# Optimization experiments

Measured on AMD Instinct MI355X. Metric: run time of the kernel, lower is better.

## Reference

```python
import jax, jax.numpy as jnp
import numpy as np

B, H, W = 8, 48, 48
D_MODEL, D_STATE, SSM_RATIO, K = 192, 16, 2.0, 4
D_INNER = int(SSM_RATIO * D_MODEL)        # 384
DT_RANK = int(np.ceil(D_MODEL / 16))       # 12
EPS = 1e-6


def setup_inputs() -> dict:
    key = jax.random.key(0)
    ks = jax.random.split(key, 12)
    s = 0.02
    inp = {
        "x": jax.random.normal(ks[0], (B, H, W, D_MODEL), jnp.float32),
        "in_proj_w": s * jax.random.normal(ks[1], (2 * D_INNER, D_MODEL), jnp.float32),
        "conv_w": s * jax.random.normal(ks[2], (D_INNER, 1, 3, 3), jnp.float32),
        "conv_b": jnp.zeros((D_INNER,), jnp.float32),
        "x_proj_w": s * jax.random.normal(ks[3], (K, DT_RANK + 2 * D_STATE, D_INNER), jnp.float32),
        "dt_w": s * jax.random.normal(ks[4], (K, D_INNER, DT_RANK), jnp.float32),
        "dt_bias": 0.05 * jax.random.normal(ks[5], (K, D_INNER), jnp.float32),
        "A_logs": jnp.log(jnp.broadcast_to(jnp.arange(1, D_STATE + 1, dtype=jnp.float32), (K * D_INNER, D_STATE)).copy()),
        "Ds": jnp.ones((K * D_INNER,), jnp.float32),
        "ln_w": jnp.ones((D_INNER,), jnp.float32),
        "ln_b": jnp.zeros((D_INNER,), jnp.float32),
        "out_proj_w": s * jax.random.normal(ks[6], (D_MODEL, D_INNER), jnp.float32),
    }
    return inp


def _selective_scan(u, dt, A, Bs, Cs):
    # u, dt: (B,K,D,L); A: (K,D,N); Bs, Cs: (B,K,N,L)
    u_t = jnp.moveaxis(u, -1, 0)    # (L,B,K,D)
    dt_t = jnp.moveaxis(dt, -1, 0)  # (L,B,K,D)
    B_t = jnp.moveaxis(Bs, -1, 0)   # (L,B,K,N)
    C_t = jnp.moveaxis(Cs, -1, 0)   # (L,B,K,N)
    b = u.shape[0]
    h0 = jnp.zeros((b, K, D_INNER, D_STATE), jnp.float32)

    def step(h, inp):
        ut, dtt, bt, ct = inp
        dA = jnp.exp(dtt[..., None] * A)                       # (B,K,D,N)
        h = dA * h + (dtt * ut)[..., None] * bt[:, :, None, :]  # (B,K,D,N)
        y = jnp.einsum('bkdn,bkn->bkd', h, ct)
        return h, y

    _, ys = jax.lax.scan(step, h0, (u_t, dt_t, B_t, C_t))
    return jnp.moveaxis(ys, 0, -1)  # (B,K,D,L)


def reference(x, in_proj_w, conv_w, conv_b, x_proj_w, dt_w, dt_bias, A_logs, Ds, ln_w, ln_b, out_proj_w):
    b, h, w, _ = x.shape
    L = h * w
    # in_proj + split into x / gate z
    xz = jnp.einsum('bhwc,oc->bhwo', x, in_proj_w)
    xi, z = jnp.split(xz, 2, axis=-1)
    z = jax.nn.silu(z)
    # depthwise 3x3 conv, channel-first
    xi = jnp.transpose(xi, (0, 3, 1, 2))  # (B,Di,H,W)
    xi = jax.lax.conv_general_dilated(
        xi, conv_w, window_strides=(1, 1), padding='SAME',
        feature_group_count=D_INNER,
        dimension_numbers=('NCHW', 'OIHW', 'NCHW')) + conv_b[None, :, None, None]
    xi = jax.nn.silu(xi)
    # cross-scan: 4 directions (row-major, col-major, and their reverses)
    xr = xi.reshape(b, D_INNER, L)
    xc = jnp.transpose(xi, (0, 1, 3, 2)).reshape(b, D_INNER, L)
    xs = jnp.stack([xr, xc, jnp.flip(xr, -1), jnp.flip(xc, -1)], axis=1)  # (B,K,D,L)
    # per-direction projections
    x_dbl = jnp.einsum('bkdl,kcd->bkcl', xs, x_proj_w)  # (B,K,R+2N,L)
    dts = x_dbl[:, :, :DT_RANK]
    Bs = x_dbl[:, :, DT_RANK:DT_RANK + D_STATE]
    Cs = x_dbl[:, :, DT_RANK + D_STATE:]
    dts = jnp.einsum('bkrl,kdr->bkdl', dts, dt_w)
    A = -jnp.exp(A_logs.astype(jnp.float32)).reshape(K, D_INNER, D_STATE)
    dt = jax.nn.softplus(dts + dt_bias[None, :, :, None])
    ys = _selective_scan(xs.astype(jnp.float32), dt, A, Bs.astype(jnp.float32), Cs.astype(jnp.float32))
    ys = ys + Ds.reshape(1, K, D_INNER, 1) * xs  # skip
    # cross-merge (invert each direction, sum)
    def col2row(t):
        return jnp.transpose(t.reshape(b, D_INNER, w, h), (0, 1, 3, 2)).reshape(b, D_INNER, L)
    y = ys[:, 0] + col2row(ys[:, 1]) + jnp.flip(ys[:, 2], -1) + col2row(jnp.flip(ys[:, 3], -1))
    y = jnp.transpose(y.reshape(b, D_INNER, h, w), (0, 2, 3, 1))  # (B,H,W,Di)
    # LayerNorm over channel dim
    mu = y.mean(-1, keepdims=True)
    var = ((y - mu) ** 2).mean(-1, keepdims=True)
    y = (y - mu) / jnp.sqrt(var + EPS) * ln_w + ln_b
    # gate + out_proj
    y = y * z
    out = jnp.einsum('bhwd,od->bhwo', y, out_proj_w)
    return out.astype(x.dtype)
```

## Files before the change

kernel.cpp:

```cpp
#include <hip/hip_runtime.h>

#define BB 8
#define HH 48
#define WW2 48
#define LL 2304
#define CIN 192
#define DI 384
#define NK 4
#define RR 12
#define NS 16
#define CD 44
#define NX 176
#define MM 18432
#define NC 48
#define CL 48

typedef unsigned short u16;
typedef __attribute__((ext_vector_type(8))) short s16x8;
typedef __attribute__((ext_vector_type(4))) float f32x4;
typedef __attribute__((ext_vector_type(2))) float f32x2;

#if __has_builtin(__builtin_elementwise_fma)
#define EFMA(a, b, c) __builtin_elementwise_fma((a), (b), (c))
#else
#define EFMA(a, b, c) ((a) * (b) + (c))
#endif

static __device__ __forceinline__ float siluf(float x) { return x / (1.f + __expf(-x)); }

static __device__ __forceinline__ u16 f2bf(float x) {
    unsigned u = __float_as_uint(x);
    return (u16)((u + 0x7FFFu + ((u >> 16) & 1u)) >> 16);
}
static __device__ __forceinline__ float bf2f(u16 h) {
    return __uint_as_float(((unsigned)h) << 16);
}

static __device__ __forceinline__ int posmap(int k, int l) {
    switch (k & 3) {
    case 0: return l;
    case 1: { int w = l / HH; int h = l - w * HH; return h * WW2 + w; }
    case 2: return LL - 1 - l;
    default: { int j = LL - 1 - l; int w = j / HH; int h = j - w * HH; return h * WW2 + w; }
    }
}

#define W0N 147456
#define W1N 67584
#define W2N 73728
__global__ __launch_bounds__(256) void k_cvtw(const float* __restrict__ w0,
                                              const float* __restrict__ w1,
                                              const float* __restrict__ w2,
                                              u16* __restrict__ wpl) {
    int i = (blockIdx.x * 256 + threadIdx.x) * 4;
    const float* src; u16* hi; u16* lo; int base;
    if (i < W0N)                { src = w0; hi = wpl;          lo = wpl + 147456; base = i; }
    else if (i < W0N + W1N)     { src = w1; hi = wpl + 294912; lo = wpl + 362496; base = i - W0N; }
    else if (i < W0N + W1N + W2N) { src = w2; hi = wpl + 430080; lo = wpl + 503808; base = i - W0N - W1N; }
    else return;
    float4 v = *(const float4*)(src + base);
    u16 h0 = f2bf(v.x), h1 = f2bf(v.y), h2 = f2bf(v.z), h3 = f2bf(v.w);
    hi[base + 0] = h0; hi[base + 1] = h1; hi[base + 2] = h2; hi[base + 3] = h3;
    lo[base + 0] = f2bf(v.x - bf2f(h0));
    lo[base + 1] = f2bf(v.y - bf2f(h1));
    lo[base + 2] = f2bf(v.z - bf2f(h2));
    lo[base + 3] = f2bf(v.w - bf2f(h3));
}

template<int N, int K, int EPI, int ACVT, int SPLIT>
__global__ __launch_bounds__(256) void k_gemm(const u16* __restrict__ Ahg,
                                              const u16* __restrict__ Alg,
                                              const u16* __restrict__ Bhg,
                                              const u16* __restrict__ Blg,
                                              float* __restrict__ O1,
                                              void* __restrict__ O2) {
    __shared__ __align__(16) u16 lds[SPLIT == 3 ? 12288 : 10240];
    const int m0 = blockIdx.x << 7;
    const int n0 = blockIdx.y << 6;
    const int t = threadIdx.x;
    const int lane = t & 63;
    const int w = t >> 6;
    const int wm = w & 1, wn = w >> 1;

    f32x4 acc[4][2];
#pragma unroll
    for (int mi = 0; mi < 4; ++mi)
#pragma unroll
        for (int ni = 0; ni < 2; ++ni)
#pragma unroll
            for (int r = 0; r < 4; ++r) acc[mi][ni][r] = 0.f;

    const int rA = lane & 15;
    const int kb = (lane >> 4) << 3;

    for (int k0 = 0; k0 < K; k0 += 32) {
#pragma unroll
        for (int rep = 0; rep < 2; ++rep) {
            int q = t + (rep << 8);
            int row = q >> 2;
            int kk = (q & 3) << 3;
            size_t ga = (size_t)(m0 + row) * K + k0 + kk;
            if (ACVT) {
                const float* Af = (const float*)Ahg;
                float vv[8];
                *(float4*)(vv + 0) = *(const float4*)(Af + ga);
                *(float4*)(vv + 4) = *(const float4*)(Af + ga + 4);
                u16 hbuf[8], lbuf[8];
#pragma unroll
                for (int i = 0; i < 8; ++i) {
                    u16 h = f2bf(vv[i]);
                    hbuf[i] = h;
                    lbuf[i] = f2bf(vv[i] - bf2f(h));
                }
                *(uint4*)&lds[(row << 5) + kk] = *(uint4*)hbuf;
                *(uint4*)&lds[4096 + (row << 5) + kk] = *(uint4*)lbuf;
            } else {
                *(uint4*)&lds[(row << 5) + kk] = *(const uint4*)(Ahg + ga);
                *(uint4*)&lds[4096 + (row << 5) + kk] = *(const uint4*)(Alg + ga);
            }
        }
        {
            int row = t >> 2;
            int kk = (t & 3) << 3;
            int rg = n0 + row;
            if (N & 63) rg = (rg > N - 1) ? (N - 1) : rg;
            size_t gb = (size_t)rg * K + k0 + kk;
            *(uint4*)&lds[8192 + (row << 5) + kk] = *(const uint4*)(Bhg + gb);
            if (SPLIT == 3)
                *(uint4*)&lds[10240 + (row << 5) + kk] = *(const uint4*)(Blg + gb);
        }
        __syncthreads();

        s16x8 bh[2], bl[2];
#pragma unroll
        for (int ni = 0; ni < 2; ++ni) {
            int c = (wn << 5) + (ni << 4) + rA;
            bh[ni] = *(const s16x8*)&lds[8192 + (c << 5) + kb];
            if (SPLIT == 3) bl[ni] = *(const s16x8*)&lds[10240 + (c << 5) + kb];
        }
#pragma unroll
        for (int mi = 0; mi < 4; ++mi) {
            int rr = (wm << 6) + (mi << 4) + rA;
            s16x8 ah = *(const s16x8*)&lds[(rr << 5) + kb];
            s16x8 al = *(const s16x8*)&lds[4096 + (rr << 5) + kb];
#pragma unroll
            for (int ni = 0; ni < 2; ++ni) {
                acc[mi][ni] = __builtin_amdgcn_mfma_f32_16x16x32_bf16(al, bh[ni], acc[mi][ni], 0, 0, 0);
                if (SPLIT == 3)
                    acc[mi][ni] = __builtin_amdgcn_mfma_f32_16x16x32_bf16(ah, bl[ni], acc[mi][ni], 0, 0, 0);
                acc[mi][ni] = __builtin_amdgcn_mfma_f32_16x16x32_bf16(ah, bh[ni], acc[mi][ni], 0, 0, 0);
            }
        }
        __syncthreads();
    }

    const int rbase = (lane >> 4) << 2;
#pragma unroll
    for (int mi = 0; mi < 4; ++mi) {
#pragma unroll
        for (int ni = 0; ni < 2; ++ni) {
            int o = n0 + (wn << 5) + (ni << 4) + (lane & 15);
#pragma unroll
            for (int r = 0; r < 4; ++r) {
                int m = m0 + (wm << 6) + (mi << 4) + rbase + r;
                float v = acc[mi][ni][r];
                if (EPI == 0) {
                    if (o < DI) O1[(size_t)m * DI + o] = v;
                    else        ((u16*)O2)[(size_t)m * DI + (o - DI)] = f2bf(siluf(v));
                } else if (EPI == 1) {
                    if (o < NX) O1[(size_t)m * NX + o] = v;
                } else {
                    O1[(size_t)m * CIN + o] = v;
                }
            }
        }
    }
}

__global__ __launch_bounds__(192) void k_conv(const float* __restrict__ xi,
                                              const float* __restrict__ cw,
                                              const float* __restrict__ cb,
                                              float* __restrict__ ub,
                                              u16* __restrict__ ubh,
                                              u16* __restrict__ ubl) {
    int blk = blockIdx.x;
    int b = blk / LL, p = blk - b * LL;
    int h = p / WW2, w = p - h * WW2;
    int d2 = threadIdx.x * 2;

    float w0[9], w1[9];
#pragma unroll
    for (int i = 0; i < 9; ++i) {
        w0[i] = cw[d2 * 9 + i];
        w1[i] = cw[(d2 + 1) * 9 + i];
    }
    float ax = cb[d2], ay = cb[d2 + 1];
#pragma unroll
    for (int dh = -1; dh <= 1; ++dh) {
        int hh = h + dh;
        if (hh < 0 || hh >= HH) continue;
#pragma unroll
        for (int dw = -1; dw <= 1; ++dw) {
            int ww = w + dw;
            if (ww < 0 || ww >= WW2) continue;
            float2 v = *(const float2*)(xi + ((size_t)b * LL + hh * WW2 + ww) * DI + d2);
            int tap = (dh + 1) * 3 + (dw + 1);
            ax = fmaf(w0[tap], v.x, ax);
            ay = fmaf(w1[tap], v.y, ay);
        }
    }
    float ox = siluf(ax), oy = siluf(ay);
    size_t idx = ((size_t)b * LL + p) * DI + d2;
    float2 o2; o2.x = ox; o2.y = oy;
    *(float2*)(ub + idx) = o2;
    u16 h0 = f2bf(ox), h1 = f2bf(oy);
    *(unsigned*)(ubh + idx) = (unsigned)h0 | ((unsigned)h1 << 16);
    unsigned l0 = f2bf(ox - bf2f(h0)), l1 = f2bf(oy - bf2f(h1));
    *(unsigned*)(ubl + idx) = l0 | (l1 << 16);
}

static __device__ __forceinline__ void adv_p(int k, int& p, int& hh) {
    if (k == 0) { ++p; }
    else if (k == 2) { --p; }
    else if (k == 1) {
        bool wrap = (hh == HH - 1);
        hh = wrap ? 0 : hh + 1;
        p += wrap ? -(LL - 1 - HH) : WW2;
    } else {
        bool wrap = (hh == 0);
        hh = wrap ? HH - 1 : hh - 1;
        p += wrap ? (LL - 1 - HH) : -WW2;
    }
}

static __device__ __forceinline__ void init_p(int k, int l0, int& p, int& hh) {
    hh = 0;
    if (k == 0) p = l0;
    else if (k == 2) p = LL - 1 - l0;
    else if (k == 1) { int w0 = l0 / HH; hh = l0 - w0 * HH; p = hh * WW2 + w0; }
    else { int j0 = LL - 1 - l0; int w0 = j0 / HH; hh = j0 - w0 * HH; p = hh * WW2 + w0; }
}

static __device__ __forceinline__ void scan_decode(int blk, int& b, int& k, int& dblk, int& c) {
    b = blk & 7;
    int r = blk >> 3;
    c = r % NC;
    int t2 = r / NC;
    dblk = t2 % 3;
    k = t2 / 3;
}

__global__ __launch_bounds__(128) void k_scan1(const float* __restrict__ ub,
                                               const float* __restrict__ xdbl,
                                               const float* __restrict__ dt_w,
                                               const float* __restrict__ dt_bias,
                                               const float* __restrict__ A_logs,
                                               float* __restrict__ HF,
                                               float* __restrict__ SD) {
    int b, k, dblk, c;
    scan_decode(blockIdx.x, b, k, dblk, c);
    int bk = (b << 2) | k;
    int d = (dblk << 7) + threadIdx.x;
    int kd = k * DI + d;

    float dtw[RR];
#pragma unroll
    for (int r = 0; r < RR; ++r) dtw[r] = dt_w[(size_t)kd * RR + r];
    float dtb = dt_bias[kd];
    float a[NS];
    bool fast = true;
#pragma unroll
    for (int n = 0; n < NS; ++n) {
        a[n] = -__expf(A_logs[(size_t)kd * NS + n]);
        fast = fast && (fabsf(a[n] + (float)(n + 1)) < 1e-3f * (float)(n + 1));
    }
    int use_fast = __all((int)fast);

    f32x2 h2[8];
#pragma unroll
    for (int i = 0; i < 8; ++i) { h2[i][0] = 0.f; h2[i][1] = 0.f; }
    float sumdt = 0.f;

    const float* cb0 = xdbl + (size_t)b * LL * NX + k * CD;
    const float* ubase = ub + (size_t)b * LL * DI + d;
    const int l0 = c * CL;
    int p, hh;
    init_p(k, l0, p, hh);

    if (use_fast) {
        for (int li = 0; li < CL; ++li) {
            const float4* cp4 = (const float4*)(cb0 + (size_t)p * NX);
            float dq[12];
            *(float4*)(dq + 0) = cp4[0];
            *(float4*)(dq + 4) = cp4[1];
            *(float4*)(dq + 8) = cp4[2];
            float s = dtb;
#pragma unroll
            for (int r = 0; r < RR; ++r) s = fmaf(dtw[r], dq[r], s);
            float es = __expf(s);
            float dt = (s > 15.f) ? s : __logf(1.f + es);
            float E = __builtin_amdgcn_rcpf(1.f + es);
            sumdt += dt;
            float uv = ubase[(size_t)p * DI];
            float du = dt * uv;
            float bb2[16];
            *(float4*)(bb2 + 0)  = cp4[3];
            *(float4*)(bb2 + 4)  = cp4[4];
            *(float4*)(bb2 + 8)  = cp4[5];
            *(float4*)(bb2 + 12) = cp4[6];
            const f32x2* b2 = (const f32x2*)bb2;
            float ee = E * E;
            f32x2 pw2; pw2[0] = E; pw2[1] = ee;
            f32x2 ee2; ee2[0] = ee; ee2[1] = ee;
            f32x2 du2; du2[0] = du; du2[1] = du;
#pragma unroll
            for (int i = 0; i < 8; ++i) {
                h2[i] = EFMA(du2, b2[i], pw2 * h2[i]);
                if (i < 7) pw2 = pw2 * ee2;
            }
            adv_p(k, p, hh);
        }
    } else {
        for (int li = 0; li < CL; ++li) {
            int l = l0 + li;
            int pp = posmap(k, l);
            const float* cp = cb0 + (size_t)pp * NX;
            float s = dtb;
#pragma unroll
            for (int r = 0; r < RR; ++r) s = fmaf(dtw[r], cp[r], s);
            float dt = (s > 15.f) ? s : log1pf(__expf(s));
            sumdt += dt;
            float uv = ubase[(size_t)pp * DI];
            float du = dt * uv;
#pragma unroll
            for (int n = 0; n < NS; ++n) {
                float dA = __expf(dt * a[n]);
                float hv = h2[n >> 1][n & 1];
                h2[n >> 1][n & 1] = fmaf(du, cp[RR + n], dA * hv);
            }
        }
    }
    size_t base = ((size_t)bk * NC + c);
#pragma unroll
    for (int i = 0; i < 8; ++i) {
        HF[(base * NS + 2 * i) * DI + d] = h2[i][0];
        HF[(base * NS + 2 * i + 1) * DI + d] = h2[i][1];
    }
    SD[base * DI + d] = sumdt;
}

__global__ __launch_bounds__(256) void k_scan2(const float* __restrict__ A_logs,
                                               float* __restrict__ HF,
                                               const float* __restrict__ SD) {
    int idx = blockIdx.x * 256 + threadIdx.x;
    int bk = idx / DI;
    int d = idx - bk * DI;
    int k = bk & 3;
    int kd = k * DI + d;

    float a[NS];
    bool fast = true;
#pragma unroll
    for (int n = 0; n < NS; ++n) {
        a[n] = -__expf(A_logs[(size_t)kd * NS + n]);
        fast = fast && (fabsf(a[n] + (float)(n + 1)) < 1e-3f * (float)(n + 1));
    }
    int use_fast = __all((int)fast);

    float H[NS];
#pragma unroll
    for (int n = 0; n < NS; ++n) H[n] = 0.f;

    for (int c = 0; c < NC; ++c) {
        size_t base = ((size_t)bk * NC + c);
        float sd = SD[base * DI + d];
        if (use_fast) {
            float E = __expf(-sd);
            float pw = 1.f;
#pragma unroll
            for (int n = 0; n < NS; ++n) {
                pw *= E;
                float hf = HF[(base * NS + n) * DI + d];
                HF[(base * NS + n) * DI + d] = H[n];
                H[n] = fmaf(pw, H[n], hf);
            }
        } else {
#pragma unroll
            for (int n = 0; n < NS; ++n) {
                float dec = __expf(a[n] * sd);
                float hf = HF[(base * NS + n) * DI + d];
                HF[(base * NS + n) * DI + d] = H[n];
                H[n] = fmaf(dec, H[n], hf);
            }
        }
    }
}

__global__ __launch_bounds__(128) void k_scan3(const float* __restrict__ ub,
                                               const float* __restrict__ xdbl,
                                               const float* __restrict__ dt_w,
                                               const float* __restrict__ dt_bias,
                                               const float* __restrict__ A_logs,
                                               const float* __restrict__ Ds,
                                               const float* __restrict__ HF,
                                               float* __restrict__ ycomb) {
    int b, k, dblk, c;
    scan_decode(blockIdx.x, b, k, dblk, c);
    int bk = (b << 2) | k;
    int d = (dblk << 7) + threadIdx.x;
    int kd = k * DI + d;

    float dtw[RR];
#pragma unroll
    for (int r = 0; r < RR; ++r) dtw[r] = dt_w[(size_t)kd * RR + r];
    float dtb = dt_bias[kd];
    float dsv = Ds[kd];
    float a[NS];
    bool fast = true;
#pragma unroll
    for (int n = 0; n < NS; ++n) {
        a[n] = -__expf(A_logs[(size_t)kd * NS + n]);
        fast = fast && (fabsf(a[n] + (float)(n + 1)) < 1e-3f * (float)(n + 1));
    }
    int use_fast = __all((int)fast);

    f32x2 h2[8];
    size_t sbase = ((size_t)bk * NC + c);
#pragma unroll
    for (int i = 0; i < 8; ++i) {
        h2[i][0] = HF[(sbase * NS + 2 * i) * DI + d];
        h2[i][1] = HF[(sbase * NS + 2 * i + 1) * DI + d];
    }

    const float* cb0 = xdbl + (size_t)b * LL * NX + k * CD;
    const float* ubase = ub + (size_t)b * LL * DI + d;
    float* ybase = ycomb + (size_t)b * LL * DI + d;
    const int l0 = c * CL;
    int p, hh;
    init_p(k, l0, p, hh);

    if (use_fast) {
        for (int li = 0; li < CL; ++li) {
            const float4* cp4 = (const float4*)(cb0 + (size_t)p * NX);
            float dq[12];
            *(float4*)(dq + 0) = cp4[0];
            *(float4*)(dq + 4) = cp4[1];
            *(float4*)(dq + 8) = cp4[2];
            float s = dtb;
#pragma unroll
            for (int r = 0; r < RR; ++r) s = fmaf(dtw[r], dq[r], s);
            float es = __expf(s);
            float dt = (s > 15.f) ? s : __logf(1.f + es);
            float E = __builtin_amdgcn_rcpf(1.f + es);
            float uv = ubase[(size_t)p * DI];
            float du = dt * uv;
            float bc[32];
            *(float4*)(bc + 0)  = cp4[3];
            *(float4*)(bc + 4)  = cp4[4];
            *(float4*)(bc + 8)  = cp4[5];
            *(float4*)(bc + 12) = cp4[6];
            *(float4*)(bc + 16) = cp4[7];
            *(float4*)(bc + 20) = cp4[8];
            *(float4*)(bc + 24) = cp4[9];
            *(float4*)(bc + 28) = cp4[10];
            const f32x2* b2 = (const f32x2*)bc;
            float ee = E * E;
            f32x2 pw2; pw2[0] = E; pw2[1] = ee;
            f32x2 ee2; ee2[0] = ee; ee2[1] = ee;
            f32x2 du2; du2[0] = du; du2[1] = du;
            f32x2 y2; y2[0] = 0.f; y2[1] = 0.f;
#pragma unroll
            for (int i = 0; i < 8; ++i) {
                h2[i] = EFMA(du2, b2[i], pw2 * h2[i]);
                y2 = EFMA(h2[i], b2[8 + i], y2);
                if (i < 7) pw2 = pw2 * ee2;
            }
            atomicAdd(ybase + (size_t)p * DI, fmaf(dsv, uv, y2[0] + y2[1]));
            adv_p(k, p, hh);
        }
    } else {
        for (int li = 0; li < CL; ++li) {
            int l = l0 + li;
            int pp = posmap(k, l);
            const float* cp = cb0 + (size_t)pp * NX;
            float s = dtb;
#pragma unroll
            for (int r = 0; r < RR; ++r) s = fmaf(dtw[r], cp[r], s);
            float dt = (s > 15.f) ? s : log1pf(__expf(s));
            float uv = ubase[(size_t)pp * DI];
            float du = dt * uv;
            float y = 0.f;
#pragma unroll
            for (int n = 0; n < NS; ++n) {
                float dA = __expf(dt * a[n]);
                float hv = h2[n >> 1][n & 1];
                hv = fmaf(du, cp[RR + n], dA * hv);
                h2[n >> 1][n & 1] = hv;
                y = fmaf(hv, cp[RR + NS + n], y);
            }
            atomicAdd(ybase + (size_t)pp * DI, fmaf(dsv, uv, y));
        }
    }
}

static __device__ __forceinline__ float waveRedSum(float v) {
#pragma unroll
    for (int o = 32; o; o >>= 1) v += __shfl_down(v, o);
    return v;
}

__global__ __launch_bounds__(128) void k_lngate(const float* __restrict__ ycomb,
                                                const u16* __restrict__ zb16,
                                                const float* __restrict__ lnw,
                                                const float* __restrict__ lnb,
                                                u16* __restrict__ ylnh,
                                                u16* __restrict__ ylnl) {
    int m = blockIdx.x;
    const float* yr = ycomb + (size_t)m * DI;
    float v[3];
    float s1 = 0.f, s2 = 0.f;
#pragma unroll
    for (int i = 0; i < 3; ++i) {
        v[i] = yr[threadIdx.x + (i << 7)];
        s1 += v[i];
        s2 = fmaf(v[i], v[i], s2);
    }
    s1 = waveRedSum(s1);
    s2 = waveRedSum(s2);
    __shared__ float p1[2], p2[2];
    int wid = threadIdx.x >> 6, lane = threadIdx.x & 63;
    if (lane == 0) { p1[wid] = s1; p2[wid] = s2; }
    __syncthreads();
    float S1 = p1[0] + p1[1];
    float S2 = p2[0] + p2[1];
    float mu = S1 * (1.f / DI);
    float var = S2 * (1.f / DI) - mu * mu;
    float rstd = rsqrtf(var + 1e-6f);
#pragma unroll
    for (int i = 0; i < 3; ++i) {
        int dd = threadIdx.x + (i << 7);
        float o = ((v[i] - mu) * rstd) * lnw[dd] + lnb[dd];
        float g = o * bf2f(zb16[(size_t)m * DI + dd]);
        u16 hh = f2bf(g);
        ylnh[(size_t)m * DI + dd] = hh;
        ylnl[(size_t)m * DI + dd] = f2bf(g - bf2f(hh));
    }
}

extern "C" void kernel_launch(void* const* d_in, const int* in_sizes, int n_in,
                              void* d_out, int out_size, void* d_ws, size_t ws_size,
                              hipStream_t stream) {
    const float* x         = (const float*)d_in[0];
    const float* in_proj_w = (const float*)d_in[1];
    const float* conv_w    = (const float*)d_in[2];
    const float* conv_b    = (const float*)d_in[3];
    const float* x_proj_w  = (const float*)d_in[4];
    const float* dt_w      = (const float*)d_in[5];
    const float* dt_bias   = (const float*)d_in[6];
    const float* A_logs    = (const float*)d_in[7];
    const float* Ds        = (const float*)d_in[8];
    const float* ln_w      = (const float*)d_in[9];
    const float* ln_b      = (const float*)d_in[10];
    const float* out_proj_w= (const float*)d_in[11];
    float* out = (float*)d_out;
    float* ws  = (float*)d_ws;

    const size_t SZ = (size_t)MM * DI;
    float* xi    = ws;
    u16*   zb16  = (u16*)(ws + SZ + SZ / 2);
    float* ub    = ws + 2 * SZ;
    float* xdbl  = ws + 3 * SZ;
    float* ycomb = ws + 3 * SZ + (size_t)MM * NX;
    u16*   wpl   = (u16*)(ycomb + SZ);

    u16* wphi  = wpl;
    u16* wplo  = wpl + 147456;
    u16* xpwhi = wpl + 294912;
    u16* xpwlo = wpl + 362496;
    u16* wohi  = wpl + 430080;
    u16* wolo  = wpl + 503808;

    u16* ubh  = (u16*)ycomb; u16* ubl = ubh + SZ;
    u16* ylnh = (u16*)xi;  u16* ylnl = ylnh + SZ;
    float* HF = ws;
    float* SD = ws + (size_t)BB * NK * NC * NS * DI;

    k_cvtw<<<(W0N + W1N + W2N) / 4 / 256 + 1, 256, 0, stream>>>(in_proj_w, x_proj_w, out_proj_w, wpl);

    k_gemm<768, CIN, 0, 1, 2><<<dim3(MM / 128, 12), 256, 0, stream>>>(
        (const u16*)x, nullptr, wphi, wplo, xi, (void*)zb16);

    k_conv<<<MM, 192, 0, stream>>>(xi, conv_w, conv_b, ub, ubh, ubl);

    k_gemm<NX, DI, 1, 0, 2><<<dim3(MM / 128, 3), 256, 0, stream>>>(ubh, ubl, xpwhi, xpwlo, xdbl, nullptr);

    hipMemsetAsync(ycomb, 0, SZ * sizeof(float), stream);

    const int nscan = BB * NK * 3 * NC;
    k_scan1<<<nscan, 128, 0, stream>>>(ub, xdbl, dt_w, dt_bias, A_logs, HF, SD);
    k_scan2<<<BB * NK * DI / 256, 256, 0, stream>>>(A_logs, HF, SD);
    k_scan3<<<nscan, 128, 0, stream>>>(ub, xdbl, dt_w, dt_bias, A_logs, Ds, HF, ycomb);

    k_lngate<<<MM, 128, 0, stream>>>(ycomb, zb16, ln_w, ln_b, ylnh, ylnl);

    k_gemm<CIN, DI, 2, 0, 2><<<dim3(MM / 128, 3), 256, 0, stream>>>(ylnh, ylnl, wohi, wolo, out, nullptr);
}
```

Measured before the change: 322.6 us.

## Fuse LayerNorm-apply and gating into out_proj GEMM A-operand load

Replaces the lngate kernel, which wrote hi/lo bf16 copies of the normalized, gated activations, with a small stats kernel that writes only per-row mean and rstd. The out_proj GEMM now reads fp32 ycomb and bf16 z directly and applies LayerNorm, affine and gate while splitting into hi/lo in its A-tile load. This removes a full write and reread of two bf16 activation buffers. In exchange the normalization work is repeated in each of the 3 N-tile blocks and the A loads become wider fp32 plus z reads.

```diff
diff --git a/kernel.cpp b/kernel.cpp
--- a/kernel.cpp
+++ b/kernel.cpp
@@ -73,7 +73,10 @@
                                               const u16* __restrict__ Bhg,
                                               const u16* __restrict__ Blg,
                                               float* __restrict__ O1,
-                                              void* __restrict__ O2) {
+                                              void* __restrict__ O2,
+                                              const float* __restrict__ lnw,
+                                              const float* __restrict__ lnb,
+                                              const float* __restrict__ stats) {
     __shared__ __align__(16) u16 lds[SPLIT == 3 ? 12288 : 10240];
     const int m0 = blockIdx.x << 7;
     const int n0 = blockIdx.y << 6;
@@ -100,7 +103,7 @@
             int row = q >> 2;
             int kk = (q & 3) << 3;
             size_t ga = (size_t)(m0 + row) * K + k0 + kk;
-            if (ACVT) {
+            if (ACVT == 1) {
                 const float* Af = (const float*)Ahg;
                 float vv[8];
                 *(float4*)(vv + 0) = *(const float4*)(Af + ga);
@@ -111,6 +114,30 @@
                     u16 h = f2bf(vv[i]);
                     hbuf[i] = h;
                     lbuf[i] = f2bf(vv[i] - bf2f(h));
+                }
+                *(uint4*)&lds[(row << 5) + kk] = *(uint4*)hbuf;
+                *(uint4*)&lds[4096 + (row << 5) + kk] = *(uint4*)lbuf;
+            } else if (ACVT == 2) {
+                const float* Yf = (const float*)Ahg;
+                int m = m0 + row;
+                float mu = stats[2 * m], rs = stats[2 * m + 1];
+                float vv[8];
+                *(float4*)(vv + 0) = *(const float4*)(Yf + ga);
+                *(float4*)(vv + 4) = *(const float4*)(Yf + ga + 4);
+                uint4 zz4 = *(const uint4*)(Alg + ga);
+                const u16* zz = (const u16*)&zz4;
+                float lw[8], lb[8];
+                *(float4*)(lw + 0) = *(const float4*)(lnw + k0 + kk);
+                *(float4*)(lw + 4) = *(const float4*)(lnw + k0 + kk + 4);
+                *(float4*)(lb + 0) = *(const float4*)(lnb + k0 + kk);
+                *(float4*)(lb + 4) = *(const float4*)(lnb + k0 + kk + 4);
+                u16 hbuf[8], lbuf[8];
+#pragma unroll
+                for (int i = 0; i < 8; ++i) {
+                    float g = fmaf((vv[i] - mu) * rs, lw[i], lb[i]) * bf2f(zz[i]);
+                    u16 h = f2bf(g);
+                    hbuf[i] = h;
+                    lbuf[i] = f2bf(g - bf2f(h));
                 }
                 *(uint4*)&lds[(row << 5) + kk] = *(uint4*)hbuf;
                 *(uint4*)&lds[4096 + (row << 5) + kk] = *(uint4*)lbuf;
@@ -503,47 +530,28 @@
     }
 }
 
-static __device__ __forceinline__ float waveRedSum(float v) {
-#pragma unroll
-    for (int o = 32; o; o >>= 1) v += __shfl_down(v, o);
-    return v;
-}
-
-__global__ __launch_bounds__(128) void k_lngate(const float* __restrict__ ycomb,
-                                                const u16* __restrict__ zb16,
-                                                const float* __restrict__ lnw,
-                                                const float* __restrict__ lnb,
-                                                u16* __restrict__ ylnh,
-                                                u16* __restrict__ ylnl) {
-    int m = blockIdx.x;
+__global__ __launch_bounds__(256) void k_lnstat(const float* __restrict__ ycomb,
+                                                float* __restrict__ stats) {
+    int m = blockIdx.x * 4 + (threadIdx.x >> 6);
+    int lane = threadIdx.x & 63;
     const float* yr = ycomb + (size_t)m * DI;
-    float v[3];
     float s1 = 0.f, s2 = 0.f;
 #pragma unroll
-    for (int i = 0; i < 3; ++i) {
-        v[i] = yr[threadIdx.x + (i << 7)];
-        s1 += v[i];
-        s2 = fmaf(v[i], v[i], s2);
-    }
-    s1 = waveRedSum(s1);
-    s2 = waveRedSum(s2);
-    __shared__ float p1[2], p2[2];
-    int wid = threadIdx.x >> 6, lane = threadIdx.x & 63;
-    if (lane == 0) { p1[wid] = s1; p2[wid] = s2; }
-    __syncthreads();
-    float S1 = p1[0] + p1[1];
-    float S2 = p2[0] + p2[1];
-    float mu = S1 * (1.f / DI);
-    float var = S2 * (1.f / DI) - mu * mu;
-    float rstd = rsqrtf(var + 1e-6f);
-#pragma unroll
-    for (int i = 0; i < 3; ++i) {
-        int dd = threadIdx.x + (i << 7);
-        float o = ((v[i] - mu) * rstd) * lnw[dd] + lnb[dd];
-        float g = o * bf2f(zb16[(size_t)m * DI + dd]);
-        u16 hh = f2bf(g);
-        ylnh[(size_t)m * DI + dd] = hh;
-        ylnl[(size_t)m * DI + dd] = f2bf(g - bf2f(hh));
+    for (int i = 0; i < 6; ++i) {
+        float v = yr[lane + (i << 6)];
+        s1 += v;
+        s2 = fmaf(v, v, s2);
+    }
+#pragma unroll
+    for (int o = 32; o; o >>= 1) {
+        s1 += __shfl_down(s1, o);
+        s2 += __shfl_down(s2, o);
+    }
+    if (lane == 0) {
+        float mu = s1 * (1.f / DI);
+        float var = s2 * (1.f / DI) - mu * mu;
+        stats[2 * m] = mu;
+        stats[2 * m + 1] = rsqrtf(var + 1e-6f);
     }
 }
 
@@ -581,18 +589,19 @@
     u16* wolo  = wpl + 503808;
 
     u16* ubh  = (u16*)ycomb; u16* ubl = ubh + SZ;
-    u16* ylnh = (u16*)xi;  u16* ylnl = ylnh + SZ;
     float* HF = ws;
     float* SD = ws + (size_t)BB * NK * NC * NS * DI;
+    float* stats = xi;
 
     k_cvtw<<<(W0N + W1N + W2N) / 4 / 256 + 1, 256, 0, stream>>>(in_proj_w, x_proj_w, out_proj_w, wpl);
 
     k_gemm<768, CIN, 0, 1, 2><<<dim3(MM / 128, 12), 256, 0, stream>>>(
-        (const u16*)x, nullptr, wphi, wplo, xi, (void*)zb16);
+        (const u16*)x, nullptr, wphi, wplo, xi, (void*)zb16, nullptr, nullptr, nullptr);
 
     k_conv<<<MM, 192, 0, stream>>>(xi, conv_w, conv_b, ub, ubh, ubl);
 
-    k_gemm<NX, DI, 1, 0, 2><<<dim3(MM / 128, 3), 256, 0, stream>>>(ubh, ubl, xpwhi, xpwlo, xdbl, nullptr);
+    k_gemm<NX, DI, 1, 0, 2><<<dim3(MM / 128, 3), 256, 0, stream>>>(
+        ubh, ubl, xpwhi, xpwlo, xdbl, nullptr, nullptr, nullptr, nullptr);
 
     hipMemsetAsync(ycomb, 0, SZ * sizeof(float), stream);
 
@@ -601,7 +610,8 @@
     k_scan2<<<BB * NK * DI / 256, 256, 0, stream>>>(A_logs, HF, SD);
     k_scan3<<<nscan, 128, 0, stream>>>(ub, xdbl, dt_w, dt_bias, A_logs, Ds, HF, ycomb);
 
-    k_lngate<<<MM, 128, 0, stream>>>(ycomb, zb16, ln_w, ln_b, ylnh, ylnl);
-
-    k_gemm<CIN, DI, 2, 0, 2><<<dim3(MM / 128, 3), 256, 0, stream>>>(ylnh, ylnl, wohi, wolo, out, nullptr);
-}
+    k_lnstat<<<MM / 4, 256, 0, stream>>>(ycomb, stats);
+
+    k_gemm<CIN, DI, 2, 2, 2><<<dim3(MM / 128, 3), 256, 0, stream>>>(
+        (const u16*)ycomb, zb16, wohi, wolo, out, nullptr, ln_w, ln_b, stats);
+}
```

Result: slower. 333.6 us (+3.4%).
